# Kernel tuning notes

Measured on AMD Instinct MI355X. Metric: run time of the kernel, lower is better.

The kernel has to match this reference:

```python
import jax, jax.numpy as jnp
import numpy as np

BSZ, NLVL, E, H, FFN = 8, 4, 512, 8, 2048
D = E // H
NNZ = 131072
LMAX = NNZ // BSZ  # equal per-batch counts -> static padded length
THETA = 10.0


def _layernorm(x, g, b):
    mu = x.mean(-1, keepdims=True)
    var = ((x - mu) ** 2).mean(-1, keepdims=True)
    return (x - mu) / jnp.sqrt(var + 1e-5) * g + b


def _rope(x, pos, freqs):
    # x: [N, E], pos: [N] float, freqs: [H, D/2] -> rotate interleaved pairs per head
    N = x.shape[0]
    nh, half = freqs.shape
    xr = x.reshape(N, nh, half, 2)
    ang = pos[:, None, None] * freqs[None]            # [N, H, D/2]
    c, s = jnp.cos(ang), jnp.sin(ang)
    x1, x2 = xr[..., 0], xr[..., 1]
    out = jnp.stack([x1 * c - x2 * s, x1 * s + x2 * c], axis=-1)
    return out.reshape(N, -1)


def setup_inputs() -> dict:
    key = jax.random.key(0)
    ks = jax.random.split(key, 8)
    bg = jax.random.normal(ks[0], (BSZ, NLVL, E), jnp.float32)
    feature_values = jax.random.normal(ks[1], (NNZ, E), jnp.float32)
    # coalesced sparse COO -> batch indices sorted; equal counts per batch for static shapes
    feature_batch_idx = (jnp.arange(NNZ, dtype=jnp.int32) // LMAX)
    feature_level_idx = jax.random.randint(ks[2], (NNZ,), 0, NLVL, dtype=jnp.int32)
    s = 1.0 / np.sqrt(E)
    Wq = jax.random.normal(ks[3], (E, E), jnp.float32) * s
    Wkv = jax.random.normal(ks[4], (E, 2 * E), jnp.float32) * s
    Wo = jax.random.normal(ks[5], (E, E), jnp.float32) * s
    freqs = THETA ** (-jnp.arange(D // 2, dtype=jnp.float32) * 2.0 / D)
    rope_freqs = jnp.tile(freqs[None, :], (H, 1))  # share_heads=False: per-head table
    ln_attn_g, ln_attn_b = jnp.ones(E, jnp.float32), jnp.zeros(E, jnp.float32)
    ln_ffn_g, ln_ffn_b = jnp.ones(E, jnp.float32), jnp.zeros(E, jnp.float32)
    W1 = jax.random.normal(ks[6], (E, FFN), jnp.float32) * s
    b1 = jnp.zeros(FFN, jnp.float32)
    W2 = jax.random.normal(ks[7], (FFN, E), jnp.float32) * (1.0 / np.sqrt(FFN))
    b2 = jnp.zeros(E, jnp.float32)
    return {
        'bg': bg, 'feature_values': feature_values,
        'feature_batch_idx': feature_batch_idx, 'feature_level_idx': feature_level_idx,
        'Wq': Wq, 'Wkv': Wkv, 'Wo': Wo, 'rope_freqs': rope_freqs,
        'ln_attn_g': ln_attn_g, 'ln_attn_b': ln_attn_b,
        'ln_ffn_g': ln_ffn_g, 'ln_ffn_b': ln_ffn_b,
        'W1': W1, 'b1': b1, 'W2': W2, 'b2': b2,
        'max_len': LMAX,
    }


def reference(bg, feature_values, feature_batch_idx, feature_level_idx,
              Wq, Wkv, Wo, rope_freqs, ln_attn_g, ln_attn_b,
              ln_ffn_g, ln_ffn_b, W1, b1, W2, b2, max_len):
    bsz, nlvl, e = bg.shape
    nh = rope_freqs.shape[0]
    d = e // nh
    nnz = feature_values.shape[0]

    # --- attention block (pre-norm) ---
    residual = bg
    x = _layernorm(bg, ln_attn_g, ln_attn_b)
    q = (x @ Wq).reshape(bsz * nlvl, e)
    kv = feature_values @ Wkv
    k, v = kv[:, :e], kv[:, e:]

    # RoPE on level indices (replicates original's repeat_interleave ordering: level = i // bsz)
    q_lvl = (jnp.arange(bsz * nlvl) // bsz).astype(jnp.float32)
    q = _rope(q, q_lvl, rope_freqs)
    k = _rope(k, feature_level_idx.astype(jnp.float32), rope_freqs)

    # concatenated (ragged) -> padded per batch
    counts = jax.ops.segment_sum(jnp.ones(nnz, jnp.int32), feature_batch_idx, num_segments=bsz)
    offsets = jnp.concatenate([jnp.zeros(1, jnp.int32), jnp.cumsum(counts)[:-1].astype(jnp.int32)])
    pos = jnp.arange(nnz, dtype=jnp.int32) - offsets[feature_batch_idx]
    k_pad = jnp.zeros((bsz, max_len, e), k.dtype).at[feature_batch_idx, pos].set(k)
    v_pad = jnp.zeros((bsz, max_len, e), v.dtype).at[feature_batch_idx, pos].set(v)
    pad_mask = jnp.arange(max_len)[None, :] >= counts[:, None]  # True at padding

    # SDPA
    qh = q.reshape(bsz, nlvl, nh, d).transpose(0, 2, 1, 3)
    kh = k_pad.reshape(bsz, max_len, nh, d).transpose(0, 2, 1, 3)
    vh = v_pad.reshape(bsz, max_len, nh, d).transpose(0, 2, 1, 3)
    scores = jnp.einsum('bhqd,bhkd->bhqk', qh, kh) / jnp.sqrt(jnp.asarray(d, qh.dtype))
    scores = jnp.where(pad_mask[:, None, None, :], -jnp.inf, scores)
    attn = jax.nn.softmax(scores, axis=-1)
    o = jnp.einsum('bhqk,bhkd->bhqd', attn, vh).transpose(0, 2, 1, 3).reshape(bsz, nlvl, e)
    o = o @ Wo + residual

    # --- FFN block (pre-norm) ---
    y = _layernorm(o, ln_ffn_g, ln_ffn_b)
    y = jax.nn.relu(y @ W1 + b1) @ W2 + b2
    return o + y
```

## Files before the change

### kernel.cpp

```cpp
#include <hip/hip_runtime.h>
#include <hip/hip_bf16.h>
#include <math.h>

#define BSZ 8
#define NLVL 4
#define E 512
#define H 8
#define D 64
#define FFN 2048
#define NNZ 131072
#define NQ 32
#define P32 32
#define NEGF -3.0e38f

typedef __attribute__((ext_vector_type(8))) short bf16x8;
typedef __attribute__((ext_vector_type(4))) float f32x4;

#define WS_QROT   16
#define WS_WSUM   (WS_QROT + NQ*E)
#define WS_OATT   (WS_WSUM + BSZ*P32*E)
#define WS_O2     (WS_OATT + NQ*E)
#define WS_Y      (WS_O2 + NQ*E)
#define WS_HID    (WS_Y + NQ*E)
#define WS_PART   (WS_HID + NQ*FFN)
#define WS_ML     (WS_PART + 512*P32*E)
#define WS_WALL   (WS_ML + 512*P32*2)

__device__ inline short f2bf(float x) {
    __hip_bfloat16 h = __float2bfloat16(x);
    union { __hip_bfloat16 v; short s; } u; u.v = h; return u.s;
}

__global__ void k_zero(int* wsi) {
    if (blockIdx.x == 0 && threadIdx.x < 8) wsi[threadIdx.x] = 0;
}

__global__ void k_hist(const int* __restrict__ fb, int* wsi) {
    __shared__ int h[8];
    int t = threadIdx.x;
    if (t < 8) h[t] = 0;
    __syncthreads();
    for (int j = blockIdx.x * 256 + t; j < NNZ; j += gridDim.x * 256)
        atomicAdd(&h[fb[j]], 1);
    __syncthreads();
    if (t < 8) atomicAdd(&wsi[t], h[t]);
}

__global__ void k_off(int* wsi) {
    if (threadIdx.x == 0) {
        int run = 0;
        for (int b = 0; b < 8; b++) { wsi[8 + b] = run; run += wsi[b]; }
    }
}

__global__ void k_tr(const float* __restrict__ Wkv, float* __restrict__ wkt) {
    __shared__ float tile[64][65];
    int ct = blockIdx.x & 7, et = blockIdx.x >> 3;
    int t = threadIdx.x;
    int tc = t & 63, tr = t >> 6;
#pragma unroll
    for (int i = 0; i < 16; i++) {
        int e = et * 64 + tr + i * 4;
        tile[tr + i * 4][tc] = Wkv[(size_t)e * (2 * E) + ct * 64 + tc];
    }
    __syncthreads();
#pragma unroll
    for (int i = 0; i < 16; i++) {
        int c = tr + i * 4;
        wkt[(size_t)(ct * 64 + c) * E + et * 64 + tc] = tile[tc][c];
    }
}

__global__ void k_qrot(const float* __restrict__ bg, const float* __restrict__ Wq,
                       const float* __restrict__ rf, const float* __restrict__ g,
                       const float* __restrict__ bb, float* __restrict__ ws) {
    __shared__ float xr[E];
    __shared__ float qrow[E];
    __shared__ float red[8];
    int r = blockIdx.x, t = threadIdx.x;
    float v0 = bg[r * E + t], v1 = bg[r * E + t + 256];
    float s = v0 + v1;
    for (int o = 32; o > 0; o >>= 1) s += __shfl_down(s, o, 64);
    if ((t & 63) == 0) red[t >> 6] = s;
    __syncthreads();
    if (t == 0) red[0] = (red[0] + red[1] + red[2] + red[3]) * (1.0f / E);
    __syncthreads();
    float mu = red[0];
    __syncthreads();
    float d0 = v0 - mu, d1 = v1 - mu;
    s = d0 * d0 + d1 * d1;
    for (int o = 32; o > 0; o >>= 1) s += __shfl_down(s, o, 64);
    if ((t & 63) == 0) red[t >> 6] = s;
    __syncthreads();
    if (t == 0) red[0] = rsqrtf((red[0] + red[1] + red[2] + red[3]) * (1.0f / E) + 1e-5f);
    __syncthreads();
    float rstd = red[0];
    xr[t] = d0 * rstd * g[t] + bb[t];
    xr[t + 256] = d1 * rstd * g[t + 256] + bb[t + 256];
    __syncthreads();
    for (int half = 0; half < 2; half++) {
        int c = t + half * 256;
        float acc = 0.f;
        for (int e = 0; e < E; e++) acc += xr[e] * Wq[e * E + c];
        qrow[c] = acc;
    }
    __syncthreads();
    int c0 = 2 * t, c1 = c0 + 1;
    int h = c0 >> 6, ii = (c0 & 63) >> 1;
    float freq = rf[h * 32 + ii];
    float pos = (float)(r >> 3);
    float a = pos * freq, ca = cosf(a), sa = sinf(a);
    float x1 = qrow[c0], x2 = qrow[c1];
    float* qr = ws + WS_QROT + r * E;
    qr[c0] = x1 * ca - x2 * sa;
    qr[c1] = x1 * sa + x2 * ca;
}

__global__ void k_wtil(const float* __restrict__ wkt, const float* __restrict__ rf,
                       const float* __restrict__ ws, short* __restrict__ wall) {
    __shared__ float u[D];
    int blk = blockIdx.x;
    int h = blk & 7, lvl = (blk >> 3) & 3, r = blk >> 5;
    int b = r >> 2, l = r & 3;
    int t = threadIdx.x;
    const float* qr = ws + WS_QROT + r * E + h * D;
    if (t < 32) {
        float freq = rf[h * 32 + t];
        float a = (float)lvl * freq;
        float ca = cosf(a), sa = sinf(a);
        float x1 = qr[2 * t], x2 = qr[2 * t + 1];
        u[2 * t] = x1 * ca + x2 * sa;
        u[2 * t + 1] = -x1 * sa + x2 * ca;
    }
    __syncthreads();
    float acc[8];
#pragma unroll
    for (int i = 0; i < 8; i++) acc[i] = 0.f;
    for (int c = 0; c < D; c++) {
        float uc = u[c];
        const float* wt = wkt + (size_t)(h * D + c) * E + t;
#pragma unroll
        for (int i = 0; i < 8; i++) acc[i] += wt[i * 64] * uc;
    }
    int n = lvl * 32 + l * 8 + h;
    short* wrow_out = wall + ((size_t)(b * 128 + n)) * E;
#pragma unroll
    for (int i = 0; i < 8; i++) wrow_out[t + i * 64] = f2bf(acc[i] * 0.125f);
}

#define KSTR 520
#define TSTR 40
__global__ __launch_bounds__(256, 2) void k_flash(
    const float* __restrict__ fv, const int* __restrict__ fl,
    const short* __restrict__ wall, const int* __restrict__ wsi,
    const int* __restrict__ maxlen, float* __restrict__ part, float* __restrict__ ml) {
    __shared__ short kbuf[32 * KSTR];
    __shared__ short fvT[512 * TSTR];
    __shared__ short pbuf[32 * TSTR];
    __shared__ float mbuf[4 * 32];
    __shared__ float lpart[4 * 32];

    int t = threadIdx.x;
    int w = t >> 6, lane = t & 63, col = lane & 15, quad = lane >> 4;
    int b = blockIdx.x, kc = blockIdx.y;
    int cnt = wsi[b], mlen = maxlen[0];
    int lim = cnt < mlen ? cnt : mlen;
    int off = wsi[8 + b];
    int kbase = kc * 256;
    int nv = lim - kbase; if (nv > 256) nv = 256; if (nv < 0) nv = 0;

    float m_reg[2][4], l_reg[2][4], a_reg[2][4];
#pragma unroll
    for (int mt = 0; mt < 2; mt++)
#pragma unroll
        for (int r = 0; r < 4; r++) { m_reg[mt][r] = NEGF; l_reg[mt][r] = 0.f; }

    f32x4 acc_o[2][8];
#pragma unroll
    for (int mt = 0; mt < 2; mt++)
#pragma unroll
        for (int nt = 0; nt < 8; nt++) acc_o[mt][nt] = f32x4{0.f, 0.f, 0.f, 0.f};

    const short* wallb = wall + (size_t)b * 128 * E;
    int sj = (t & 15) * 2;
    int se = (t >> 4) * 32;

    float4 pf0[8], pf1[8];
    if (nv > 0) {
        int g0 = off + kbase + sj, g1 = g0 + 1;
        if (g0 > NNZ - 1) g0 = NNZ - 1;
        if (g1 > NNZ - 1) g1 = NNZ - 1;
        const float* r0 = fv + (size_t)g0 * E + se;
        const float* r1 = fv + (size_t)g1 * E + se;
#pragma unroll
        for (int i = 0; i < 8; i++) {
            pf0[i] = *(const float4*)(r0 + i * 4);
            pf1[i] = *(const float4*)(r1 + i * 4);
        }
    }

    for (int s = 0; s < 8; s++) {
        int vs = nv - s * 32;
        if (vs <= 0) break;
        __syncthreads();
#pragma unroll
        for (int i = 0; i < 8; i++) {
            float4 x0 = pf0[i], x1 = pf1[i];
            int e = se + i * 4;
            *(__hip_bfloat162*)&kbuf[sj * KSTR + e]           = __float22bfloat162_rn(float2{x0.x, x0.y});
            *(__hip_bfloat162*)&kbuf[sj * KSTR + e + 2]       = __float22bfloat162_rn(float2{x0.z, x0.w});
            *(__hip_bfloat162*)&kbuf[(sj + 1) * KSTR + e]     = __float22bfloat162_rn(float2{x1.x, x1.y});
            *(__hip_bfloat162*)&kbuf[(sj + 1) * KSTR + e + 2] = __float22bfloat162_rn(float2{x1.z, x1.w});
            *(__hip_bfloat162*)&fvT[(e + 0) * TSTR + sj] = __float22bfloat162_rn(float2{x0.x, x1.x});
            *(__hip_bfloat162*)&fvT[(e + 1) * TSTR + sj] = __float22bfloat162_rn(float2{x0.y, x1.y});
            *(__hip_bfloat162*)&fvT[(e + 2) * TSTR + sj] = __float22bfloat162_rn(float2{x0.z, x1.z});
            *(__hip_bfloat162*)&fvT[(e + 3) * TSTR + sj] = __float22bfloat162_rn(float2{x0.w, x1.w});
        }
        if (nv - (s + 1) * 32 > 0) {
            int g0 = off + kbase + (s + 1) * 32 + sj, g1 = g0 + 1;
            if (g0 > NNZ - 1) g0 = NNZ - 1;
            if (g1 > NNZ - 1) g1 = NNZ - 1;
            const float* r0 = fv + (size_t)g0 * E + se;
            const float* r1 = fv + (size_t)g1 * E + se;
#pragma unroll
            for (int i = 0; i < 8; i++) {
                pf0[i] = *(const float4*)(r0 + i * 4);
                pf1[i] = *(const float4*)(r1 + i * 4);
            }
        }
        int kg0 = off + kbase + s * 32 + col;
        int kg1 = kg0 + 16;
        if (kg0 > NNZ - 1) kg0 = NNZ - 1;
        if (kg1 > NNZ - 1) kg1 = NNZ - 1;
        int lv0 = fl[kg0], lv1 = fl[kg1];
        bool valid0 = (s * 32 + col) < nv;
        bool valid1 = (s * 32 + 16 + col) < nv;
        bool sel0 = valid0 && (lv0 == w);
        bool sel1 = valid1 && (lv1 == w);
        __syncthreads();
        f32x4 acc_s[2][2];
#pragma unroll
        for (int mt = 0; mt < 2; mt++)
#pragma unroll
            for (int kt = 0; kt < 2; kt++) acc_s[mt][kt] = f32x4{0.f, 0.f, 0.f, 0.f};
        {
            const short* wr0 = wallb + (size_t)(w * 32 + col) * E + quad * 8;
            const short* wr1 = wr0 + (size_t)16 * E;
            const short* kb0 = &kbuf[col * KSTR + quad * 8];
            const short* kb1 = &kbuf[(16 + col) * KSTR + quad * 8];
            __builtin_amdgcn_s_setprio(1);
#pragma unroll
            for (int ks = 0; ks < 16; ks++) {
                int e0 = ks * 32;
                bf16x8 A0 = *(const bf16x8*)(wr0 + e0);
                bf16x8 A1 = *(const bf16x8*)(wr1 + e0);
                bf16x8 B0 = *(const bf16x8*)(kb0 + e0);
                bf16x8 B1 = *(const bf16x8*)(kb1 + e0);
                acc_s[0][0] = __builtin_amdgcn_mfma_f32_16x16x32_bf16(A0, B0, acc_s[0][0], 0, 0, 0);
                acc_s[0][1] = __builtin_amdgcn_mfma_f32_16x16x32_bf16(A0, B1, acc_s[0][1], 0, 0, 0);
                acc_s[1][0] = __builtin_amdgcn_mfma_f32_16x16x32_bf16(A1, B0, acc_s[1][0], 0, 0, 0);
                acc_s[1][1] = __builtin_amdgcn_mfma_f32_16x16x32_bf16(A1, B1, acc_s[1][1], 0, 0, 0);
            }
            __builtin_amdgcn_s_setprio(0);
        }
#pragma unroll
        for (int mt = 0; mt < 2; mt++) {
#pragma unroll
            for (int r = 0; r < 4; r++) {
                float v0 = sel0 ? acc_s[mt][0][r] : NEGF;
                float v1 = sel1 ? acc_s[mt][1][r] : NEGF;
                float v = fmaxf(v0, v1);
#pragma unroll
                for (int msk = 1; msk < 16; msk <<= 1) v = fmaxf(v, __shfl_xor(v, msk, 16));
                if (col == 0) mbuf[w * 32 + mt * 16 + quad * 4 + r] = v;
            }
        }
        __syncthreads();
#pragma unroll
        for (int mt = 0; mt < 2; mt++)
#pragma unroll
            for (int r = 0; r < 4; r++) {
                int p = mt * 16 + quad * 4 + r;
                float mo = m_reg[mt][r];
                float mn = fmaxf(mo, fmaxf(fmaxf(mbuf[p], mbuf[32 + p]),
                                           fmaxf(mbuf[64 + p], mbuf[96 + p])));
                a_reg[mt][r] = __expf(mo - mn);
                m_reg[mt][r] = mn;
            }
#pragma unroll
        for (int mt = 0; mt < 2; mt++) {
#pragma unroll
            for (int r = 0; r < 4; r++) {
                int p = mt * 16 + quad * 4 + r;
                float ls = 0.f;
                if (sel0) {
                    float pv = __expf(acc_s[mt][0][r] - m_reg[mt][r]);
                    pbuf[p * TSTR + col] = f2bf(pv);
                    ls += pv;
                } else if (w == 0 && !valid0) {
                    pbuf[p * TSTR + col] = 0;
                }
                if (sel1) {
                    float pv = __expf(acc_s[mt][1][r] - m_reg[mt][r]);
                    pbuf[p * TSTR + 16 + col] = f2bf(pv);
                    ls += pv;
                } else if (w == 0 && !valid1) {
                    pbuf[p * TSTR + 16 + col] = 0;
                }
#pragma unroll
                for (int msk = 1; msk < 16; msk <<= 1) ls += __shfl_xor(ls, msk, 16);
                if (col == 0) lpart[w * 32 + p] = ls;
            }
        }
#pragma unroll
        for (int mt = 0; mt < 2; mt++)
#pragma unroll
            for (int nt = 0; nt < 8; nt++)
#pragma unroll
                for (int r = 0; r < 4; r++) acc_o[mt][nt][r] *= a_reg[mt][r];
        __syncthreads();
        {
            bf16x8 Ap0 = *(const bf16x8*)&pbuf[col * TSTR + quad * 8];
            bf16x8 Ap1 = *(const bf16x8*)&pbuf[(16 + col) * TSTR + quad * 8];
            const short* bt = &fvT[(size_t)(w * 128 + col) * TSTR + quad * 8];
            __builtin_amdgcn_s_setprio(1);
#pragma unroll
            for (int nt = 0; nt < 8; nt++) {
                bf16x8 Bf = *(const bf16x8*)(bt + (size_t)nt * 16 * TSTR);
                acc_o[0][nt] = __builtin_amdgcn_mfma_f32_16x16x32_bf16(Ap0, Bf, acc_o[0][nt], 0, 0, 0);
                acc_o[1][nt] = __builtin_amdgcn_mfma_f32_16x16x32_bf16(Ap1, Bf, acc_o[1][nt], 0, 0, 0);
            }
            __builtin_amdgcn_s_setprio(0);
        }
#pragma unroll
        for (int mt = 0; mt < 2; mt++)
#pragma unroll
            for (int r = 0; r < 4; r++) {
                int p = mt * 16 + quad * 4 + r;
                l_reg[mt][r] = l_reg[mt][r] * a_reg[mt][r] +
                               (lpart[p] + lpart[32 + p] + lpart[64 + p] + lpart[96 + p]);
            }
    }
    size_t pbase = ((size_t)(b * 64 + kc) * P32) * E;
#pragma unroll
    for (int mt = 0; mt < 2; mt++)
#pragma unroll
        for (int r = 0; r < 4; r++) {
            int p = mt * 16 + quad * 4 + r;
#pragma unroll
            for (int nt = 0; nt < 8; nt++) {
                int e = w * 128 + nt * 16 + col;
                part[pbase + (size_t)p * E + e] = acc_o[mt][nt][r];
            }
        }
    if (w == 0 && col == 0) {
#pragma unroll
        for (int mt = 0; mt < 2; mt++)
#pragma unroll
            for (int r = 0; r < 4; r++) {
                int p = mt * 16 + quad * 4 + r;
                size_t idx = (size_t)(b * 64 + kc) * P32 + p;
                ml[idx * 2] = m_reg[mt][r];
                ml[idx * 2 + 1] = l_reg[mt][r];
            }
    }
}

__global__ void k_merge(const float* __restrict__ part, const float* __restrict__ ml,
                        float* __restrict__ wsum) {
    __shared__ float wexp[64];
    int b = blockIdx.x >> 5, p = blockIdx.x & 31;
    int t = threadIdx.x;
    float M = NEGF;
    for (int kc = 0; kc < 64; kc++)
        M = fmaxf(M, ml[((size_t)(b * 64 + kc) * P32 + p) * 2]);
    float denom = 0.f;
    for (int kc = 0; kc < 64; kc++) {
        size_t idx = ((size_t)(b * 64 + kc) * P32 + p) * 2;
        denom += ml[idx + 1] * expf(ml[idx] - M);
    }
    if (t < 64)
        wexp[t] = expf(ml[((size_t)(b * 64 + t) * P32 + p) * 2] - M);
    __syncthreads();
    float inv = 1.0f / denom;
    for (int half = 0; half < 2; half++) {
        int e = t + half * 256;
        float acc = 0.f;
        for (int kc = 0; kc < 64; kc++)
            acc += part[((size_t)(b * 64 + kc) * P32 + p) * E + e] * wexp[kc];
        wsum[((size_t)(b * P32 + p)) * E + e] = acc * inv;
    }
}

__global__ void k_oproj(const float* __restrict__ wsum, const float* __restrict__ Wkv,
                        float* __restrict__ oatt) {
    __shared__ float Aw[NQ][E];
    int h = blockIdx.x >> 2, ct = blockIdx.x & 3;
    int t = threadIdx.x;
    {
        int rr = t >> 3, x = (t & 7) * 64;
        int row = (rr >> 2) * P32 + (rr & 3) * 8 + h;
#pragma unroll
        for (int q4 = 0; q4 < 16; q4++)
            *(float4*)&Aw[rr][x + q4 * 4] = *(const float4*)&wsum[(size_t)row * E + x + q4 * 4];
    }
    __syncthreads();
#pragma unroll
    for (int rep = 0; rep < 2; rep++) {
        int idx = rep * 256 + t;
        int rr = idx >> 4, cl = idx & 15;
        int c = h * D + ct * 16 + cl;
        float acc = 0.f;
        for (int e = 0; e < E; e++) acc += Aw[rr][e] * Wkv[(size_t)e * (2 * E) + E + c];
        oatt[rr * E + c] = acc;
    }
}

__global__ void k_wo(const float* __restrict__ oatt, const float* __restrict__ Wo,
                     const float* __restrict__ bg, float* __restrict__ o2) {
    __shared__ float Aw[NQ * E];
    int t = threadIdx.x;
#pragma unroll
    for (int q = 0; q < 16; q++) {
        int i = (q * 256 + t) * 4;
        *(float4*)&Aw[i] = *(const float4*)&oatt[i];
    }
    __syncthreads();
    int ct = blockIdx.x;
#pragma unroll
    for (int rep = 0; rep < 4; rep++) {
        int idx = rep * 256 + t;
        int rr = idx >> 5, cl = idx & 31;
        int c = ct * 32 + cl;
        float acc = bg[rr * E + c];
        for (int e = 0; e < E; e++) acc += Aw[rr * E + e] * Wo[(size_t)e * E + c];
        o2[rr * E + c] = acc;
    }
}

__global__ void k_ln2(const float* __restrict__ o2, const float* __restrict__ g,
                      const float* __restrict__ bb, float* __restrict__ y) {
    __shared__ float red[8];
    int r = blockIdx.x, t = threadIdx.x;
    float v0 = o2[r * E + t], v1 = o2[r * E + t + 256];
    float s = v0 + v1;
    for (int o = 32; o > 0; o >>= 1) s += __shfl_down(s, o, 64);
    if ((t & 63) == 0) red[t >> 6] = s;
    __syncthreads();
    if (t == 0) red[0] = (red[0] + red[1] + red[2] + red[3]) * (1.0f / E);
    __syncthreads();
    float mu = red[0];
    __syncthreads();
    float d0 = v0 - mu, d1 = v1 - mu;
    s = d0 * d0 + d1 * d1;
    for (int o = 32; o > 0; o >>= 1) s += __shfl_down(s, o, 64);
    if ((t & 63) == 0) red[t >> 6] = s;
    __syncthreads();
    if (t == 0) red[0] = rsqrtf((red[0] + red[1] + red[2] + red[3]) * (1.0f / E) + 1e-5f);
    __syncthreads();
    float rstd = red[0];
    y[r * E + t] = d0 * rstd * g[t] + bb[t];
    y[r * E + t + 256] = d1 * rstd * g[t + 256] + bb[t + 256];
}

__global__ void k_ffn1(const float* __restrict__ y, const float* __restrict__ W1,
                       const float* __restrict__ b1, float* __restrict__ hid) {
    __shared__ float Aw[NQ * E];
    int t = threadIdx.x;
#pragma unroll
    for (int q = 0; q < 16; q++) {
        int i = (q * 256 + t) * 4;
        *(float4*)&Aw[i] = *(const float4*)&y[i];
    }
    __syncthreads();
    int ft = blockIdx.x;
#pragma unroll
    for (int rep = 0; rep < 4; rep++) {
        int idx = rep * 256 + t;
        int rr = idx >> 5, fl = idx & 31;
        int f = ft * 32 + fl;
        float acc = b1[f];
        for (int e = 0; e < E; e++) acc += Aw[rr * E + e] * W1[(size_t)e * FFN + f];
        hid[rr * FFN + f] = fmaxf(acc, 0.f);
    }
}

__global__ void k_ffn2(const float* __restrict__ hid, const float* __restrict__ W2,
                       const float* __restrict__ b2, const float* __restrict__ o2,
                       float* __restrict__ out) {
    int ct = blockIdx.x;
    int t = threadIdx.x;
#pragma unroll
    for (int rep = 0; rep < 2; rep++) {
        int idx = rep * 256 + t;
        int rr = idx >> 4, cl = idx & 15;
        int c = ct * 16 + cl;
        float acc = b2[c] + o2[rr * E + c];
        for (int f = 0; f < FFN; f++) acc += hid[rr * FFN + f] * W2[(size_t)f * E + c];
        out[rr * E + c] = acc;
    }
}

extern "C" void kernel_launch(void* const* d_in, const int* in_sizes, int n_in,
                              void* d_out, int out_size, void* d_ws, size_t ws_size,
                              hipStream_t stream) {
    const float* bg  = (const float*)d_in[0];
    const float* fv  = (const float*)d_in[1];
    const int*   fb  = (const int*)d_in[2];
    const int*   fl  = (const int*)d_in[3];
    const float* Wq  = (const float*)d_in[4];
    const float* Wkv = (const float*)d_in[5];
    const float* Wo  = (const float*)d_in[6];
    const float* rf  = (const float*)d_in[7];
    const float* lag = (const float*)d_in[8];
    const float* lab = (const float*)d_in[9];
    const float* lfg = (const float*)d_in[10];
    const float* lfb = (const float*)d_in[11];
    const float* W1  = (const float*)d_in[12];
    const float* b1  = (const float*)d_in[13];
    const float* W2  = (const float*)d_in[14];
    const float* b2  = (const float*)d_in[15];
    const int* maxlen = (const int*)d_in[16];
    float* ws = (float*)d_ws;
    int* wsi = (int*)d_ws;
    short* wall = (short*)(ws + WS_WALL);
    float* wkt = ws + WS_PART;
    float* out = (float*)d_out;

    hipLaunchKernelGGL(k_zero, dim3(1), dim3(64), 0, stream, wsi);
    hipLaunchKernelGGL(k_hist, dim3(128), dim3(256), 0, stream, fb, wsi);
    hipLaunchKernelGGL(k_off, dim3(1), dim3(64), 0, stream, wsi);
    hipLaunchKernelGGL(k_tr, dim3(64), dim3(256), 0, stream, Wkv, wkt);
    hipLaunchKernelGGL(k_qrot, dim3(NQ), dim3(256), 0, stream, bg, Wq, rf, lag, lab, ws);
    hipLaunchKernelGGL(k_wtil, dim3(NQ * NLVL * H), dim3(64), 0, stream, wkt, rf, ws, wall);
    hipLaunchKernelGGL(k_flash, dim3(BSZ, 64), dim3(256), 0, stream,
                       fv, fl, wall, wsi, maxlen, ws + WS_PART, ws + WS_ML);
    hipLaunchKernelGGL(k_merge, dim3(BSZ * P32), dim3(256), 0, stream,
                       ws + WS_PART, ws + WS_ML, ws + WS_WSUM);
    hipLaunchKernelGGL(k_oproj, dim3(H * 4), dim3(256), 0, stream,
                       ws + WS_WSUM, Wkv, ws + WS_OATT);
    hipLaunchKernelGGL(k_wo, dim3(16), dim3(256), 0, stream,
                       ws + WS_OATT, Wo, bg, ws + WS_O2);
    hipLaunchKernelGGL(k_ln2, dim3(NQ), dim3(256), 0, stream,
                       ws + WS_O2, lfg, lfb, ws + WS_Y);
    hipLaunchKernelGGL(k_ffn1, dim3(FFN / 32), dim3(256), 0, stream,
                       ws + WS_Y, W1, b1, ws + WS_HID);
    hipLaunchKernelGGL(k_ffn2, dim3(E / 16), dim3(256), 0, stream,
                       ws + WS_HID, W2, b2, ws + WS_O2, out);
}
```

Measured before the change: 861.7 us.

## Split-K the tail GEMV kernels with atomics and drop flash register prefetch

The small post-attention matmuls (output projection, Wo, FFN1, FFN2) now split the reduction dimension across a second grid axis and combine partial sums with atomicAdd into zeroed buffers. This raises the block count from 16–64 to 128–512, so far more CUs stream the weights. The ReLU moves from FFN1's store to FFN2's load, and memsets are added to clear the accumulators. Separately, the flash kernel drops its register double-buffered prefetch of feature rows and loads each tile just before use, which cuts register pressure but gives up load/compute overlap. k_merge's block-index mapping is also swapped.

```diff
diff --git a/kernel.cpp b/kernel.cpp
--- a/kernel.cpp
+++ b/kernel.cpp
@@ -185,47 +185,20 @@
     int sj = (t & 15) * 2;
     int se = (t >> 4) * 32;
 
-    float4 pf0[8], pf1[8];
-    if (nv > 0) {
-        int g0 = off + kbase + sj, g1 = g0 + 1;
-        if (g0 > NNZ - 1) g0 = NNZ - 1;
-        if (g1 > NNZ - 1) g1 = NNZ - 1;
-        const float* r0 = fv + (size_t)g0 * E + se;
-        const float* r1 = fv + (size_t)g1 * E + se;
-#pragma unroll
-        for (int i = 0; i < 8; i++) {
-            pf0[i] = *(const float4*)(r0 + i * 4);
-            pf1[i] = *(const float4*)(r1 + i * 4);
-        }
-    }
-
     for (int s = 0; s < 8; s++) {
         int vs = nv - s * 32;
         if (vs <= 0) break;
-        __syncthreads();
-#pragma unroll
-        for (int i = 0; i < 8; i++) {
-            float4 x0 = pf0[i], x1 = pf1[i];
-            int e = se + i * 4;
-            *(__hip_bfloat162*)&kbuf[sj * KSTR + e]           = __float22bfloat162_rn(float2{x0.x, x0.y});
-            *(__hip_bfloat162*)&kbuf[sj * KSTR + e + 2]       = __float22bfloat162_rn(float2{x0.z, x0.w});
-            *(__hip_bfloat162*)&kbuf[(sj + 1) * KSTR + e]     = __float22bfloat162_rn(float2{x1.x, x1.y});
-            *(__hip_bfloat162*)&kbuf[(sj + 1) * KSTR + e + 2] = __float22bfloat162_rn(float2{x1.z, x1.w});
-            *(__hip_bfloat162*)&fvT[(e + 0) * TSTR + sj] = __float22bfloat162_rn(float2{x0.x, x1.x});
-            *(__hip_bfloat162*)&fvT[(e + 1) * TSTR + sj] = __float22bfloat162_rn(float2{x0.y, x1.y});
-            *(__hip_bfloat162*)&fvT[(e + 2) * TSTR + sj] = __float22bfloat162_rn(float2{x0.z, x1.z});
-            *(__hip_bfloat162*)&fvT[(e + 3) * TSTR + sj] = __float22bfloat162_rn(float2{x0.w, x1.w});
-        }
-        if (nv - (s + 1) * 32 > 0) {
-            int g0 = off + kbase + (s + 1) * 32 + sj, g1 = g0 + 1;
+        float4 x0[8], x1[8];
+        {
+            int g0 = off + kbase + s * 32 + sj, g1 = g0 + 1;
             if (g0 > NNZ - 1) g0 = NNZ - 1;
             if (g1 > NNZ - 1) g1 = NNZ - 1;
             const float* r0 = fv + (size_t)g0 * E + se;
             const float* r1 = fv + (size_t)g1 * E + se;
 #pragma unroll
             for (int i = 0; i < 8; i++) {
-                pf0[i] = *(const float4*)(r0 + i * 4);
-                pf1[i] = *(const float4*)(r1 + i * 4);
+                x0[i] = *(const float4*)(r0 + i * 4);
+                x1[i] = *(const float4*)(r1 + i * 4);
             }
         }
         int kg0 = off + kbase + s * 32 + col;
@@ -237,6 +210,20 @@
         bool valid1 = (s * 32 + 16 + col) < nv;
         bool sel0 = valid0 && (lv0 == w);
         bool sel1 = valid1 && (lv1 == w);
+        __syncthreads();
+#pragma unroll
+        for (int i = 0; i < 8; i++) {
+            float4 v0 = x0[i], v1 = x1[i];
+            int e = se + i * 4;
+            *(__hip_bfloat162*)&kbuf[sj * KSTR + e]           = __float22bfloat162_rn(float2{v0.x, v0.y});
+            *(__hip_bfloat162*)&kbuf[sj * KSTR + e + 2]       = __float22bfloat162_rn(float2{v0.z, v0.w});
+            *(__hip_bfloat162*)&kbuf[(sj + 1) * KSTR + e]     = __float22bfloat162_rn(float2{v1.x, v1.y});
+            *(__hip_bfloat162*)&kbuf[(sj + 1) * KSTR + e + 2] = __float22bfloat162_rn(float2{v1.z, v1.w});
+            *(__hip_bfloat162*)&fvT[(e + 0) * TSTR + sj] = __float22bfloat162_rn(float2{v0.x, v1.x});
+            *(__hip_bfloat162*)&fvT[(e + 1) * TSTR + sj] = __float22bfloat162_rn(float2{v0.y, v1.y});
+            *(__hip_bfloat162*)&fvT[(e + 2) * TSTR + sj] = __float22bfloat162_rn(float2{v0.z, v1.z});
+            *(__hip_bfloat162*)&fvT[(e + 3) * TSTR + sj] = __float22bfloat162_rn(float2{v0.w, v1.w});
+        }
         __syncthreads();
         f32x4 acc_s[2][2];
 #pragma unroll
@@ -369,7 +356,7 @@
 __global__ void k_merge(const float* __restrict__ part, const float* __restrict__ ml,
                         float* __restrict__ wsum) {
     __shared__ float wexp[64];
-    int b = blockIdx.x >> 5, p = blockIdx.x & 31;
+    int b = blockIdx.x & 7, p = blockIdx.x >> 3;
     int t = threadIdx.x;
     float M = NEGF;
     for (int kc = 0; kc < 64; kc++)
@@ -394,47 +381,51 @@
 
 __global__ void k_oproj(const float* __restrict__ wsum, const float* __restrict__ Wkv,
                         float* __restrict__ oatt) {
-    __shared__ float Aw[NQ][E];
-    int h = blockIdx.x >> 2, ct = blockIdx.x & 3;
-    int t = threadIdx.x;
+    __shared__ float Aw[32][64];
+    int ct = blockIdx.x, kc = blockIdx.y, t = threadIdx.x;
+    int h = ct >> 1;
     {
-        int rr = t >> 3, x = (t & 7) * 64;
-        int row = (rr >> 2) * P32 + (rr & 3) * 8 + h;
-#pragma unroll
-        for (int q4 = 0; q4 < 16; q4++)
-            *(float4*)&Aw[rr][x + q4 * 4] = *(const float4*)&wsum[(size_t)row * E + x + q4 * 4];
-    }
-    __syncthreads();
-#pragma unroll
-    for (int rep = 0; rep < 2; rep++) {
-        int idx = rep * 256 + t;
-        int rr = idx >> 4, cl = idx & 15;
-        int c = h * D + ct * 16 + cl;
-        float acc = 0.f;
-        for (int e = 0; e < E; e++) acc += Aw[rr][e] * Wkv[(size_t)e * (2 * E) + E + c];
-        oatt[rr * E + c] = acc;
-    }
-}
-
-__global__ void k_wo(const float* __restrict__ oatt, const float* __restrict__ Wo,
-                     const float* __restrict__ bg, float* __restrict__ o2) {
-    __shared__ float Aw[NQ * E];
-    int t = threadIdx.x;
-#pragma unroll
-    for (int q = 0; q < 16; q++) {
-        int i = (q * 256 + t) * 4;
-        *(float4*)&Aw[i] = *(const float4*)&oatt[i];
-    }
-    __syncthreads();
-    int ct = blockIdx.x;
+        int rr = t >> 3, kk = (t & 7) * 8;
+        int wrow = (rr >> 2) * P32 + (rr & 3) * 8 + h;
+        const float* src = &wsum[(size_t)wrow * E + kc * 64 + kk];
+        *(float4*)&Aw[rr][kk]     = *(const float4*)src;
+        *(float4*)&Aw[rr][kk + 4] = *(const float4*)(src + 4);
+    }
+    __syncthreads();
 #pragma unroll
     for (int rep = 0; rep < 4; rep++) {
         int idx = rep * 256 + t;
         int rr = idx >> 5, cl = idx & 31;
         int c = ct * 32 + cl;
-        float acc = bg[rr * E + c];
-        for (int e = 0; e < E; e++) acc += Aw[rr * E + e] * Wo[(size_t)e * E + c];
-        o2[rr * E + c] = acc;
+        float acc = 0.f;
+        const float* wp = &Wkv[(size_t)(kc * 64) * (2 * E) + E + c];
+#pragma unroll
+        for (int k = 0; k < 64; k++) acc += Aw[rr][k] * wp[(size_t)k * (2 * E)];
+        atomicAdd(&oatt[rr * E + c], acc);
+    }
+}
+
+__global__ void k_wo(const float* __restrict__ oatt, const float* __restrict__ Wo,
+                     const float* __restrict__ bg, float* __restrict__ o2) {
+    __shared__ float Aw[32][64];
+    int ct = blockIdx.x, kc = blockIdx.y, t = threadIdx.x;
+    {
+        int rr = t >> 3, kk = (t & 7) * 8;
+        const float* src = &oatt[(size_t)rr * E + kc * 64 + kk];
+        *(float4*)&Aw[rr][kk]     = *(const float4*)src;
+        *(float4*)&Aw[rr][kk + 4] = *(const float4*)(src + 4);
+    }
+    __syncthreads();
+#pragma unroll
+    for (int rep = 0; rep < 4; rep++) {
+        int idx = rep * 256 + t;
+        int rr = idx >> 5, cl = idx & 31;
+        int c = ct * 32 + cl;
+        float acc = (kc == 0) ? bg[rr * E + c] : 0.f;
+        const float* wp = &Wo[(size_t)(kc * 64) * E + c];
+#pragma unroll
+        for (int k = 0; k < 64; k++) acc += Aw[rr][k] * wp[(size_t)k * E];
+        atomicAdd(&o2[rr * E + c], acc);
     }
 }
 
@@ -465,39 +456,56 @@
 
 __global__ void k_ffn1(const float* __restrict__ y, const float* __restrict__ W1,
                        const float* __restrict__ b1, float* __restrict__ hid) {
-    __shared__ float Aw[NQ * E];
-    int t = threadIdx.x;
-#pragma unroll
-    for (int q = 0; q < 16; q++) {
-        int i = (q * 256 + t) * 4;
-        *(float4*)&Aw[i] = *(const float4*)&y[i];
-    }
-    __syncthreads();
-    int ft = blockIdx.x;
+    __shared__ float Aw[32][64];
+    int ft = blockIdx.x, kc = blockIdx.y, t = threadIdx.x;
+    {
+        int rr = t >> 3, kk = (t & 7) * 8;
+        const float* src = &y[(size_t)rr * E + kc * 64 + kk];
+        *(float4*)&Aw[rr][kk]     = *(const float4*)src;
+        *(float4*)&Aw[rr][kk + 4] = *(const float4*)(src + 4);
+    }
+    __syncthreads();
 #pragma unroll
     for (int rep = 0; rep < 4; rep++) {
         int idx = rep * 256 + t;
-        int rr = idx >> 5, fl = idx & 31;
-        int f = ft * 32 + fl;
-        float acc = b1[f];
-        for (int e = 0; e < E; e++) acc += Aw[rr * E + e] * W1[(size_t)e * FFN + f];
-        hid[rr * FFN + f] = fmaxf(acc, 0.f);
+        int rr = idx >> 5, fcol = idx & 31;
+        int f = ft * 32 + fcol;
+        float acc = (kc == 0) ? b1[f] : 0.f;
+        const float* wp = &W1[(size_t)(kc * 64) * FFN + f];
+#pragma unroll
+        for (int k = 0; k < 64; k++) acc += Aw[rr][k] * wp[(size_t)k * FFN];
+        atomicAdd(&hid[rr * FFN + f], acc);
     }
 }
 
 __global__ void k_ffn2(const float* __restrict__ hid, const float* __restrict__ W2,
                        const float* __restrict__ b2, const float* __restrict__ o2,
                        float* __restrict__ out) {
-    int ct = blockIdx.x;
-    int t = threadIdx.x;
-#pragma unroll
-    for (int rep = 0; rep < 2; rep++) {
+    __shared__ float Hs[32][128];
+    int ct = blockIdx.x, kc = blockIdx.y, t = threadIdx.x;
+    {
+        int rr = t >> 3, kk = (t & 7) * 16;
+        const float* src = &hid[(size_t)rr * FFN + kc * 128 + kk];
+#pragma unroll
+        for (int j = 0; j < 4; j++) {
+            float4 v = *(const float4*)(src + j * 4);
+            Hs[rr][kk + j * 4 + 0] = fmaxf(v.x, 0.f);
+            Hs[rr][kk + j * 4 + 1] = fmaxf(v.y, 0.f);
+            Hs[rr][kk + j * 4 + 2] = fmaxf(v.z, 0.f);
+            Hs[rr][kk + j * 4 + 3] = fmaxf(v.w, 0.f);
+        }
+    }
+    __syncthreads();
+#pragma unroll
+    for (int rep = 0; rep < 4; rep++) {
         int idx = rep * 256 + t;
-        int rr = idx >> 4, cl = idx & 15;
-        int c = ct * 16 + cl;
-        float acc = b2[c] + o2[rr * E + c];
-        for (int f = 0; f < FFN; f++) acc += hid[rr * FFN + f] * W2[(size_t)f * E + c];
-        out[rr * E + c] = acc;
+        int rr = idx >> 5, cl = idx & 31;
+        int c = ct * 32 + cl;
+        float acc = (kc == 0) ? (b2[c] + o2[rr * E + c]) : 0.f;
+        const float* wp = &W2[(size_t)(kc * 128) * E + c];
+#pragma unroll
+        for (int k = 0; k < 128; k++) acc += Hs[rr][k] * wp[(size_t)k * E];
+        atomicAdd(&out[rr * E + c], acc);
     }
 }
 
@@ -527,6 +535,9 @@
     float* wkt = ws + WS_PART;
     float* out = (float*)d_out;
 
+    hipMemsetAsync(ws + WS_OATT, 0, (size_t)(WS_PART - WS_OATT) * sizeof(float), stream);
+    hipMemsetAsync(d_out, 0, (size_t)NQ * E * sizeof(float), stream);
+
     hipLaunchKernelGGL(k_zero, dim3(1), dim3(64), 0, stream, wsi);
     hipLaunchKernelGGL(k_hist, dim3(128), dim3(256), 0, stream, fb, wsi);
     hipLaunchKernelGGL(k_off, dim3(1), dim3(64), 0, stream, wsi);
@@ -537,14 +548,14 @@
                        fv, fl, wall, wsi, maxlen, ws + WS_PART, ws + WS_ML);
     hipLaunchKernelGGL(k_merge, dim3(BSZ * P32), dim3(256), 0, stream,
                        ws + WS_PART, ws + WS_ML, ws + WS_WSUM);
-    hipLaunchKernelGGL(k_oproj, dim3(H * 4), dim3(256), 0, stream,
+    hipLaunchKernelGGL(k_oproj, dim3(16, 8), dim3(256), 0, stream,
                        ws + WS_WSUM, Wkv, ws + WS_OATT);
-    hipLaunchKernelGGL(k_wo, dim3(16), dim3(256), 0, stream,
+    hipLaunchKernelGGL(k_wo, dim3(16, 8), dim3(256), 0, stream,
                        ws + WS_OATT, Wo, bg, ws + WS_O2);
     hipLaunchKernelGGL(k_ln2, dim3(NQ), dim3(256), 0, stream,
                        ws + WS_O2, lfg, lfb, ws + WS_Y);
-    hipLaunchKernelGGL(k_ffn1, dim3(FFN / 32), dim3(256), 0, stream,
+    hipLaunchKernelGGL(k_ffn1, dim3(64, 8), dim3(256), 0, stream,
                        ws + WS_Y, W1, b1, ws + WS_HID);
-    hipLaunchKernelGGL(k_ffn2, dim3(E / 16), dim3(256), 0, stream,
+    hipLaunchKernelGGL(k_ffn2, dim3(16, 16), dim3(256), 0, stream,
                        ws + WS_HID, W2, b2, ws + WS_O2, out);
 }
```

Result: faster. 763.2 us (-11.4%).
